# Kernel tuning notes

Hardware: AMD Instinct MI355X
Metric: run time of the kernel (lower is better)

## Reference

```python
import jax, jax.numpy as jnp
from jax import lax
import numpy as np

MB, N, QST, EPS = 512, 25, 11, 1e-5

def _coords():
    i = np.arange(25)
    # faithful to python3 true division: (i/5 - 2)/2.0, (i%5 - 2)/2.0
    c = np.stack([(i / 5 - 2) / 2.0, (i % 5 - 2) / 2.0], axis=-1).astype(np.float32)
    return jnp.asarray(c)  # [25, 2]

def _conv_bn(x, w, b, g, beta):
    # Conv2d(k=3, stride=2, pad=1) -> ReLU -> BatchNorm (training-mode batch stats)
    y = lax.conv_general_dilated(x, w, (2, 2), [(1, 1), (1, 1)],
                                 dimension_numbers=('NCHW', 'OIHW', 'NCHW'))
    y = jax.nn.relu(y + b[None, :, None, None])
    mean = y.mean(axis=(0, 2, 3), keepdims=True)
    var = y.var(axis=(0, 2, 3), keepdims=True)
    return (y - mean) * jax.lax.rsqrt(var + EPS) * g[None, :, None, None] + beta[None, :, None, None]

def setup_inputs() -> dict:
    key = jax.random.key(0)
    ks = jax.random.split(key, 20)
    w = lambda k, s: jax.random.normal(k, s, jnp.float32) * 0.05
    inp = {
        'img': jax.random.normal(ks[0], (MB, 3, 75, 75), jnp.float32),
        'qst': jax.random.normal(ks[1], (MB, QST), jnp.float32),
        'c1w': w(ks[2], (24, 3, 3, 3)),  'c1b': jnp.zeros((24,)), 'bn1g': jnp.ones((24,)), 'bn1b': jnp.zeros((24,)),
        'c2w': w(ks[3], (24, 24, 3, 3)), 'c2b': jnp.zeros((24,)), 'bn2g': jnp.ones((24,)), 'bn2b': jnp.zeros((24,)),
        'c3w': w(ks[4], (24, 24, 3, 3)), 'c3b': jnp.zeros((24,)), 'bn3g': jnp.ones((24,)), 'bn3b': jnp.zeros((24,)),
        'c4w': w(ks[5], (24, 24, 3, 3)), 'c4b': jnp.zeros((24,)), 'bn4g': jnp.ones((24,)), 'bn4b': jnp.zeros((24,)),
        'gw1': w(ks[6], (256, 63)),  'gb1': jnp.zeros((256,)),
        'gw2': w(ks[7], (256, 256)), 'gb2': jnp.zeros((256,)),
        'gw3': w(ks[8], (256, 256)), 'gb3': jnp.zeros((256,)),
        'gw4': w(ks[9], (256, 256)), 'gb4': jnp.zeros((256,)),
        'fw1': w(ks[10], (256, 256)), 'fb1': jnp.zeros((256,)),
        'fw2': w(ks[11], (256, 256)), 'fb2': jnp.zeros((256,)),
        'fw3': w(ks[12], (10, 256)),  'fb3': jnp.zeros((10,)),
    }
    return inp

def reference(img, qst, c1w, c1b, bn1g, bn1b, c2w, c2b, bn2g, bn2b,
              c3w, c3b, bn3g, bn3b, c4w, c4b, bn4g, bn4b,
              gw1, gb1, gw2, gb2, gw3, gb3, gw4, gb4,
              fw1, fb1, fw2, fb2, fw3, fb3):
    x = _conv_bn(img, c1w, c1b, bn1g, bn1b)
    x = _conv_bn(x, c2w, c2b, bn2g, bn2b)
    x = _conv_bn(x, c3w, c3b, bn3g, bn3b)
    x = _conv_bn(x, c4w, c4b, bn4g, bn4b)  # [mb, 24, 5, 5]
    mb, C = x.shape[0], x.shape[1]
    n = x.shape[2] * x.shape[3]
    xf = x.reshape(mb, C, n).transpose(0, 2, 1)              # [mb, N, 24]
    coord = jnp.broadcast_to(_coords()[None], (mb, n, 2))
    xf = jnp.concatenate([xf, coord], axis=-1)               # [mb, N, 26]
    qrep = jnp.broadcast_to(qst[:, None, :], (mb, n, QST))
    xj = jnp.concatenate([xf, qrep], axis=-1)                # [mb, N, 37]
    # pair[b,a,c] = [xf[b,c], xf[b,a], qst[b]]  (x_i varies over axis 2, x_j over axis 1)
    pair = jnp.concatenate([
        jnp.broadcast_to(xf[:, None, :, :], (mb, n, n, xf.shape[-1])),
        jnp.broadcast_to(xj[:, :, None, :], (mb, n, n, xj.shape[-1])),
    ], axis=-1)                                              # [mb, N, N, 63]
    h = pair.reshape(mb * n * n, -1)
    for w, b in ((gw1, gb1), (gw2, gb2), (gw3, gb3), (gw4, gb4)):
        h = jax.nn.relu(h @ w.T + b)
    xg = h.reshape(mb, n * n, 256).sum(axis=1)               # sum pooling over pairs
    y = jax.nn.relu(xg @ fw1.T + fb1)
    y = jax.nn.relu(y @ fw2.T + fb2)   # dropout treated as identity (eval mode)
    y = y @ fw3.T + fb3
    return jax.nn.log_softmax(y, axis=-1)
```

## Files before the change

### kernel.cpp

```cpp
#include <hip/hip_runtime.h>

typedef __bf16 bf16_t;
typedef __bf16 bf16x8 __attribute__((ext_vector_type(8)));
typedef __bf16 bf16x4 __attribute__((ext_vector_type(4)));
typedef float f32x16 __attribute__((ext_vector_type(16)));

#define MB 512
#define GROWS 96
#define GT_PER_B 7

template <int CIN, int HIN, int WIN, int HOUT, int WOUT, bool HASBN>
__global__ __launch_bounds__(256) void conv_v4(const float* __restrict__ in,
                                               const float* __restrict__ wT,
                                               const float* __restrict__ bias,
                                               const float* __restrict__ statsIn,
                                               const float* __restrict__ gIn,
                                               const float* __restrict__ bIn, float invcntIn,
                                               float* __restrict__ out,
                                               float* __restrict__ statsOut)
{
    __shared__ float red[4 * 48];
    const int NPOS = HOUT * WOUT;
    int idx = blockIdx.x * 256 + threadIdx.x;
    int n = idx / NPOS, pos = idx - n * NPOS;
    int oh = pos / WOUT, ow = pos - oh * WOUT;

    int off[9];
    bool vld[9];
#pragma unroll
    for (int kh = 0; kh < 3; ++kh) {
        int ih = 2 * oh - 1 + kh;
        bool vh = (unsigned)ih < (unsigned)HIN;
        int ihc = vh ? ih : 0;
#pragma unroll
        for (int kw = 0; kw < 3; ++kw) {
            int iw = 2 * ow - 1 + kw;
            bool vw = (unsigned)iw < (unsigned)WIN;
            vld[kh * 3 + kw] = vh && vw;
            off[kh * 3 + kw] = ihc * WIN + (vw ? iw : 0);
        }
    }

    float acc[24];
#pragma unroll
    for (int c = 0; c < 24; ++c) acc[c] = 0.f;

    const float* srcBase = in + (size_t)n * CIN * HIN * WIN;
#pragma unroll 1
    for (int ci = 0; ci < CIN; ++ci) {
        float sc, sh;
        if (HASBN) {
            float mean = statsIn[ci * 2] * invcntIn;
            float var  = statsIn[ci * 2 + 1] * invcntIn - mean * mean;
            sc = gIn[ci] * rsqrtf(var + 1e-5f);
            sh = bIn[ci] - mean * sc;
        } else { sc = 1.f; sh = 0.f; }
        const float* src = srcBase + ci * HIN * WIN;
        float iv[9];
#pragma unroll
        for (int t = 0; t < 9; ++t) {
            float raw = src[off[t]];
            iv[t] = vld[t] ? fmaf(raw, sc, sh) : 0.f;
        }
        const float* wp = wT + ci * 9 * 24;
#pragma unroll
        for (int t = 0; t < 9; ++t) {
#pragma unroll
            for (int c4 = 0; c4 < 6; ++c4) {
                float4 w4 = *(const float4*)(wp + t * 24 + c4 * 4);
                acc[c4 * 4 + 0] = fmaf(iv[t], w4.x, acc[c4 * 4 + 0]);
                acc[c4 * 4 + 1] = fmaf(iv[t], w4.y, acc[c4 * 4 + 1]);
                acc[c4 * 4 + 2] = fmaf(iv[t], w4.z, acc[c4 * 4 + 2]);
                acc[c4 * 4 + 3] = fmaf(iv[t], w4.w, acc[c4 * 4 + 3]);
            }
        }
    }

    int wv = threadIdx.x >> 6, lane = threadIdx.x & 63;
#pragma unroll
    for (int c = 0; c < 24; ++c) {
        float v = fmaxf(acc[c] + bias[c], 0.f);
        out[((size_t)(n * 24 + c) * HOUT + oh) * WOUT + ow] = v;
        float s1 = v, s2 = v * v;
#pragma unroll
        for (int o = 1; o < 64; o <<= 1) {
            s1 += __shfl_xor(s1, o);
            s2 += __shfl_xor(s2, o);
        }
        if (lane == 0) { red[wv * 48 + c * 2] = s1; red[wv * 48 + c * 2 + 1] = s2; }
    }
    __syncthreads();
    if (threadIdx.x < 48) {
        float t = red[threadIdx.x] + red[48 + threadIdx.x] + red[96 + threadIdx.x] + red[144 + threadIdx.x];
        atomicAdd(&statsOut[threadIdx.x], t);
    }
}

__global__ void build_features(const float* __restrict__ y4, const float* __restrict__ stats4,
                               const float* __restrict__ g4, const float* __restrict__ b4,
                               const float* __restrict__ qst,
                               bf16_t* __restrict__ xf26, bf16_t* __restrict__ qstb)
{
    int idx = blockIdx.x * 256 + threadIdx.x;
    if (idx < MB * 11) qstb[idx] = (bf16_t)qst[idx];
    if (idx >= MB * 25) return;
    int b = idx / 25, p = idx % 25;
    const float invcnt = 1.f / (MB * 25);
#pragma unroll
    for (int ch = 0; ch < 24; ++ch) {
        float mean = stats4[ch * 2] * invcnt;
        float var  = stats4[ch * 2 + 1] * invcnt - mean * mean;
        float s    = g4[ch] * rsqrtf(var + 1e-5f);
        float v    = s * y4[(b * 24 + ch) * 25 + p] + (b4[ch] - mean * s);
        xf26[idx * 26 + ch] = (bf16_t)v;
    }
    xf26[idx * 26 + 24] = (bf16_t)((p / 5.0f - 2.0f) * 0.5f);
    xf26[idx * 26 + 25] = (bf16_t)(((float)(p % 5) - 2.0f) * 0.5f);
}

__device__ __forceinline__ void frag256(int idx, const float* __restrict__ gw, bf16_t* __restrict__ Wf)
{
    int j = idx & 7, lane = (idx >> 3) & 63, ks = (idx >> 9) & 15, nt = idx >> 13;
    int n = nt * 32 + (lane & 31), k = ks * 16 + (lane >> 5) * 8 + j;
    Wf[idx] = (bf16_t)gw[n * 256 + k];
}

__global__ void prep_weights(const float* __restrict__ gw1, const float* __restrict__ gw2,
                             const float* __restrict__ gw3, const float* __restrict__ gw4,
                             const float* __restrict__ fw1, const float* __restrict__ fw2,
                             const float* __restrict__ c1w, const float* __restrict__ c2w,
                             const float* __restrict__ c3w, const float* __restrict__ c4w,
                             bf16_t* __restrict__ W1f, bf16_t* __restrict__ W2f,
                             bf16_t* __restrict__ W3f, bf16_t* __restrict__ W4f,
                             float* __restrict__ fw1T, float* __restrict__ fw2T,
                             float* __restrict__ wT1, float* __restrict__ wT2,
                             float* __restrict__ wT3, float* __restrict__ wT4)
{
    int idx = blockIdx.x * 256 + threadIdx.x;
    if (idx < 16384) {
        int j = idx & 7, lane = (idx >> 3) & 63, ks = (idx >> 9) & 3, nt = idx >> 11;
        int n = nt * 32 + (lane & 31), k = ks * 16 + (lane >> 5) * 8 + j;
        W1f[idx] = (k < 63) ? (bf16_t)gw1[n * 63 + k] : (bf16_t)0.0f;
        return;
    }
    idx -= 16384;
    if (idx < 65536) { frag256(idx, gw2, W2f); return; }
    idx -= 65536;
    if (idx < 65536) { frag256(idx, gw3, W3f); return; }
    idx -= 65536;
    if (idx < 65536) { frag256(idx, gw4, W4f); return; }
    idx -= 65536;
    if (idx < 65536) { int k = idx >> 8, nn = idx & 255; fw1T[idx] = fw1[nn * 256 + k]; return; }
    idx -= 65536;
    if (idx < 65536) { int k = idx >> 8, nn = idx & 255; fw2T[idx] = fw2[nn * 256 + k]; return; }
    idx -= 65536;
    if (idx < 648)   { int k = idx / 24, co = idx - k * 24; wT1[idx] = c1w[co * 27 + k]; return; }
    idx -= 648;
    if (idx < 5184)  { int k = idx / 24, co = idx - k * 24; wT2[idx] = c2w[co * 216 + k]; return; }
    idx -= 5184;
    if (idx < 5184)  { int k = idx / 24, co = idx - k * 24; wT3[idx] = c3w[co * 216 + k]; return; }
    idx -= 5184;
    if (idx < 5184)  { int k = idx / 24, co = idx - k * 24; wT4[idx] = c4w[co * 216 + k]; return; }
}

template <int NKS>
__device__ __forceinline__ void g_layer(const bf16_t* hs, const bf16_t* __restrict__ Wf,
                                        int wid, int lane, f32x16 acc[3][2])
{
    int m31 = lane & 31, half = lane >> 5;
#pragma unroll
    for (int mt = 0; mt < 3; ++mt)
#pragma unroll
        for (int nt = 0; nt < 2; ++nt) acc[mt][nt] = (f32x16)(0.f);
#pragma unroll
    for (int ks = 0; ks < NKS; ++ks) {
        int kc = ks * 2 + half;
        bf16x8 hf[3];
#pragma unroll
        for (int mt = 0; mt < 3; ++mt) {
            int m = mt * 32 + m31;
            hf[mt] = *(const bf16x8*)(hs + m * 256 + ((kc ^ m31) << 3));
        }
        bf16x8 wf[2];
#pragma unroll
        for (int nt = 0; nt < 2; ++nt)
            wf[nt] = *(const bf16x8*)(Wf + (size_t)(((wid * 2 + nt) * NKS + ks) * 64 + lane) * 8);
#pragma unroll
        for (int nt = 0; nt < 2; ++nt)
#pragma unroll
            for (int mt = 0; mt < 3; ++mt)
                acc[mt][nt] = __builtin_amdgcn_mfma_f32_32x32x16_bf16(wf[nt], hf[mt], acc[mt][nt], 0, 0, 0);
    }
}

__device__ __forceinline__ void g_store(bf16_t* hs, const float* __restrict__ bias,
                                        int wid, int lane, f32x16 acc[3][2])
{
    int m31 = lane & 31, half = lane >> 5;
#pragma unroll
    for (int mt = 0; mt < 3; ++mt) {
        int m = mt * 32 + m31;
#pragma unroll
        for (int nt = 0; nt < 2; ++nt) {
            int nbase = (wid * 2 + nt) * 32;
#pragma unroll
            for (int g = 0; g < 4; ++g) {
                int n0 = nbase + g * 8 + half * 4;
                float4 bv = *(const float4*)(bias + n0);
                bf16x4 v;
                v[0] = (bf16_t)fmaxf(acc[mt][nt][g * 4 + 0] + bv.x, 0.f);
                v[1] = (bf16_t)fmaxf(acc[mt][nt][g * 4 + 1] + bv.y, 0.f);
                v[2] = (bf16_t)fmaxf(acc[mt][nt][g * 4 + 2] + bv.z, 0.f);
                v[3] = (bf16_t)fmaxf(acc[mt][nt][g * 4 + 3] + bv.w, 0.f);
                int chunk = n0 >> 3;
                *(bf16x4*)(hs + m * 256 + ((chunk ^ m31) << 3) + (half << 2)) = v;
            }
        }
    }
}

__global__ void __launch_bounds__(256, 3)
g_mlp(const bf16_t* __restrict__ xf26, const bf16_t* __restrict__ qstb,
      const bf16_t* __restrict__ W1f, const bf16_t* __restrict__ W2f,
      const bf16_t* __restrict__ W3f, const bf16_t* __restrict__ W4f,
      const float* __restrict__ b1, const float* __restrict__ b2,
      const float* __restrict__ b3, const float* __restrict__ b4,
      float* __restrict__ xg)
{
    __shared__ __align__(16) bf16_t hs[GROWS * 256];
    int b    = blockIdx.x / GT_PER_B;
    int tile = blockIdx.x % GT_PER_B;
    int tid  = threadIdx.x;

    for (int i = tid; i < GROWS * 8; i += 256) {
        int m = i >> 3, c = i & 7;
        int p = tile * GROWS + m;
        bf16x8 v;
        if (p < 625) {
            int a = p / 25, cp = p - a * 25;
            const bf16_t* f1 = xf26 + (b * 25 + cp) * 26;
            const bf16_t* f2 = xf26 + (b * 25 + a) * 26;
            const bf16_t* f3 = qstb + b * 11;
#pragma unroll
            for (int j = 0; j < 8; ++j) {
                int col = c * 8 + j;
                bf16_t u = (bf16_t)0.0f;
                if (col < 26) u = f1[col];
                else if (col < 52) u = f2[col - 26];
                else if (col < 63) u = f3[col - 52];
                v[j] = u;
            }
        } else {
#pragma unroll
            for (int j = 0; j < 8; ++j) v[j] = (bf16_t)0.0f;
        }
        *(bf16x8*)(hs + m * 256 + ((c ^ (m & 31)) << 3)) = v;
    }
    __syncthreads();

    int wid = tid >> 6, lane = tid & 63;
    int m31 = lane & 31, half = lane >> 5;
    f32x16 acc[3][2];

    g_layer<4>(hs, W1f, wid, lane, acc);
    __syncthreads(); g_store(hs, b1, wid, lane, acc); __syncthreads();
    g_layer<16>(hs, W2f, wid, lane, acc);
    __syncthreads(); g_store(hs, b2, wid, lane, acc); __syncthreads();
    g_layer<16>(hs, W3f, wid, lane, acc);
    __syncthreads(); g_store(hs, b3, wid, lane, acc); __syncthreads();
    g_layer<16>(hs, W4f, wid, lane, acc);

#pragma unroll
    for (int nt = 0; nt < 2; ++nt) {
        int nbase = (wid * 2 + nt) * 32;
        float bf[16];
#pragma unroll
        for (int r = 0; r < 16; ++r)
            bf[r] = b4[nbase + (r & 3) + 8 * (r >> 2) + 4 * half];
        f32x16 t = (f32x16)(0.f);
#pragma unroll
        for (int mt = 0; mt < 3; ++mt) {
            int p = tile * GROWS + mt * 32 + m31;
            if (p < 625) {
#pragma unroll
                for (int r = 0; r < 16; ++r)
                    t[r] += fmaxf(acc[mt][nt][r] + bf[r], 0.f);
            }
        }
#pragma unroll
        for (int off = 1; off < 32; off <<= 1) {
#pragma unroll
            for (int r = 0; r < 16; ++r) t[r] += __shfl_xor(t[r], off);
        }
        if (m31 == 0) {
#pragma unroll
            for (int r = 0; r < 16; ++r) {
                int nn = nbase + (r & 3) + 8 * (r >> 2) + 4 * half;
                atomicAdd(&xg[b * 256 + nn], t[r]);
            }
        }
    }
}

__global__ void f_mlp(const float* __restrict__ xg, const float* __restrict__ fw1T, const float* __restrict__ fb1,
                      const float* __restrict__ fw2T, const float* __restrict__ fb2,
                      const float* __restrict__ fw3, const float* __restrict__ fb3,
                      float* __restrict__ out)
{
    __shared__ float xa[256], xb[256], lg[10];
    int b = blockIdx.x, t = threadIdx.x;
    xa[t] = xg[b * 256 + t];
    __syncthreads();
    float a = fb1[t];
    for (int k = 0; k < 256; ++k) a += fw1T[k * 256 + t] * xa[k];
    xb[t] = fmaxf(a, 0.f);
    __syncthreads();
    a = fb2[t];
    for (int k = 0; k < 256; ++k) a += fw2T[k * 256 + t] * xb[k];
    xa[t] = fmaxf(a, 0.f);
    __syncthreads();
    if (t < 10) {
        float s = fb3[t];
        for (int k = 0; k < 256; ++k) s += fw3[t * 256 + k] * xa[k];
        lg[t] = s;
    }
    __syncthreads();
    if (t == 0) {
        float m = lg[0];
        for (int i = 1; i < 10; ++i) m = fmaxf(m, lg[i]);
        float s = 0.f;
        for (int i = 0; i < 10; ++i) s += expf(lg[i] - m);
        float ls = m + logf(s);
        for (int i = 0; i < 10; ++i) out[b * 10 + i] = lg[i] - ls;
    }
}

extern "C" void kernel_launch(void* const* d_in, const int* in_sizes, int n_in,
                              void* d_out, int out_size, void* d_ws, size_t ws_size,
                              hipStream_t stream)
{
    (void)in_sizes; (void)n_in; (void)out_size; (void)ws_size;
    const float* img  = (const float*)d_in[0];
    const float* qst  = (const float*)d_in[1];
    const float* c1w  = (const float*)d_in[2];
    const float* c1b  = (const float*)d_in[3];
    const float* bn1g = (const float*)d_in[4];
    const float* bn1b = (const float*)d_in[5];
    const float* c2w  = (const float*)d_in[6];
    const float* c2b  = (const float*)d_in[7];
    const float* bn2g = (const float*)d_in[8];
    const float* bn2b = (const float*)d_in[9];
    const float* c3w  = (const float*)d_in[10];
    const float* c3b  = (const float*)d_in[11];
    const float* bn3g = (const float*)d_in[12];
    const float* bn3b = (const float*)d_in[13];
    const float* c4w  = (const float*)d_in[14];
    const float* c4b  = (const float*)d_in[15];
    const float* bn4g = (const float*)d_in[16];
    const float* bn4b = (const float*)d_in[17];
    const float* gw1  = (const float*)d_in[18];
    const float* gb1  = (const float*)d_in[19];
    const float* gw2  = (const float*)d_in[20];
    const float* gb2  = (const float*)d_in[21];
    const float* gw3  = (const float*)d_in[22];
    const float* gb3  = (const float*)d_in[23];
    const float* gw4  = (const float*)d_in[24];
    const float* gb4  = (const float*)d_in[25];
    const float* fw1  = (const float*)d_in[26];
    const float* fb1  = (const float*)d_in[27];
    const float* fw2  = (const float*)d_in[28];
    const float* fb2  = (const float*)d_in[29];
    const float* fw3  = (const float*)d_in[30];
    const float* fb3  = (const float*)d_in[31];

    const int Y1 = 512 * 24 * 38 * 38;
    const int Y2 = 512 * 24 * 19 * 19;
    const int Y3 = 512 * 24 * 10 * 10;
    const int Y4 = 512 * 24 * 5 * 5;

    float* fp = (float*)d_ws;
    float* y1    = fp;  fp += Y1;
    float* y2    = fp;  fp += Y2;
    float* y3    = fp;  fp += Y3;
    float* y4    = fp;  fp += Y4;
    float* stats = fp;  fp += 192;
    float* xg    = fp;  fp += 512 * 256;
    float* fw1T  = fp;  fp += 65536;
    float* fw2T  = fp;  fp += 65536;
    float* wT1   = fp;  fp += 648;
    float* wT2   = fp;  fp += 5184;
    float* wT3   = fp;  fp += 5184;
    float* wT4   = fp;  fp += 5184;
    bf16_t* bp   = (bf16_t*)fp;
    bf16_t* xf26 = bp;  bp += 512 * 25 * 26;
    bf16_t* qstb = bp;  bp += 512 * 11;
    bf16_t* W1f  = bp;  bp += 16384;
    bf16_t* W2f  = bp;  bp += 65536;
    bf16_t* W3f  = bp;  bp += 65536;
    bf16_t* W4f  = bp;  bp += 65536;

    hipMemsetAsync(stats, 0, 192 * sizeof(float), stream);
    hipMemsetAsync(xg, 0, 512 * 256 * sizeof(float), stream);

    prep_weights<<<1408, 256, 0, stream>>>(gw1, gw2, gw3, gw4, fw1, fw2, c1w, c2w, c3w, c4w,
                                           W1f, W2f, W3f, W4f, fw1T, fw2T,
                                           wT1, wT2, wT3, wT4);

    conv_v4<3, 75, 75, 38, 38, false><<<2888, 256, 0, stream>>>(
        img, wT1, c1b, nullptr, nullptr, nullptr, 0.f, y1, stats + 0);

    conv_v4<24, 38, 38, 19, 19, true><<<722, 256, 0, stream>>>(
        y1, wT2, c2b, stats + 0, bn1g, bn1b, 1.f / (512.f * 1444.f), y2, stats + 48);

    conv_v4<24, 19, 19, 10, 10, true><<<200, 256, 0, stream>>>(
        y2, wT3, c3b, stats + 48, bn2g, bn2b, 1.f / (512.f * 361.f), y3, stats + 96);

    conv_v4<24, 10, 10, 5, 5, true><<<50, 256, 0, stream>>>(
        y3, wT4, c4b, stats + 96, bn3g, bn3b, 1.f / (512.f * 100.f), y4, stats + 144);

    build_features<<<50, 256, 0, stream>>>(y4, stats + 144, bn4g, bn4b, qst, xf26, qstb);

    g_mlp<<<512 * GT_PER_B, 256, 0, stream>>>(xf26, qstb, W1f, W2f, W3f, W4f,
                                              gb1, gb2, gb3, gb4, xg);

    f_mlp<<<512, 256, 0, stream>>>(xg, fw1T, fb1, fw2T, fb2, fw3, fb3, (float*)d_out);
}
```

Before: 619.5 us.

## Split conv output channels across waves to quadruple conv parallelism

Each conv block now covers 64 output positions, and its four waves each compute 6 of the 24 output channels instead of one thread computing all 24. This gives four times as many blocks and fewer accumulator registers per thread, which should help the small late conv layers fill the GPU. In exchange, every input value is loaded by four waves instead of one, and more atomic stat reductions are issued.

```diff
diff --git a/kernel.cpp b/kernel.cpp
--- a/kernel.cpp
+++ b/kernel.cpp
@@ -10,18 +10,21 @@
 #define GT_PER_B 7
 
 template <int CIN, int HIN, int WIN, int HOUT, int WOUT, bool HASBN>
-__global__ __launch_bounds__(256) void conv_v4(const float* __restrict__ in,
-                                               const float* __restrict__ wT,
-                                               const float* __restrict__ bias,
-                                               const float* __restrict__ statsIn,
-                                               const float* __restrict__ gIn,
-                                               const float* __restrict__ bIn, float invcntIn,
-                                               float* __restrict__ out,
-                                               float* __restrict__ statsOut)
-{
-    __shared__ float red[4 * 48];
+__global__ __launch_bounds__(256) void conv_v4b(const float* __restrict__ in,
+                                                const float* __restrict__ wT,
+                                                const float* __restrict__ bias,
+                                                const float* __restrict__ statsIn,
+                                                const float* __restrict__ gIn,
+                                                const float* __restrict__ bIn, float invcntIn,
+                                                float* __restrict__ out,
+                                                float* __restrict__ statsOut)
+{
+    __shared__ float red[48];
     const int NPOS = HOUT * WOUT;
-    int idx = blockIdx.x * 256 + threadIdx.x;
+    int lane = threadIdx.x & 63;
+    int cg   = threadIdx.x >> 6;
+    int co0  = cg * 6;
+    int idx  = blockIdx.x * 64 + lane;
     int n = idx / NPOS, pos = idx - n * NPOS;
     int oh = pos / WOUT, ow = pos - oh * WOUT;
 
@@ -41,9 +44,9 @@
         }
     }
 
-    float acc[24];
-#pragma unroll
-    for (int c = 0; c < 24; ++c) acc[c] = 0.f;
+    float acc[6];
+#pragma unroll
+    for (int c = 0; c < 6; ++c) acc[c] = 0.f;
 
     const float* srcBase = in + (size_t)n * CIN * HIN * WIN;
 #pragma unroll 1
@@ -62,38 +65,35 @@
             float raw = src[off[t]];
             iv[t] = vld[t] ? fmaf(raw, sc, sh) : 0.f;
         }
-        const float* wp = wT + ci * 9 * 24;
+        const float* wp = wT + ci * 9 * 24 + co0;
 #pragma unroll
         for (int t = 0; t < 9; ++t) {
-#pragma unroll
-            for (int c4 = 0; c4 < 6; ++c4) {
-                float4 w4 = *(const float4*)(wp + t * 24 + c4 * 4);
-                acc[c4 * 4 + 0] = fmaf(iv[t], w4.x, acc[c4 * 4 + 0]);
-                acc[c4 * 4 + 1] = fmaf(iv[t], w4.y, acc[c4 * 4 + 1]);
-                acc[c4 * 4 + 2] = fmaf(iv[t], w4.z, acc[c4 * 4 + 2]);
-                acc[c4 * 4 + 3] = fmaf(iv[t], w4.w, acc[c4 * 4 + 3]);
-            }
-        }
-    }
-
-    int wv = threadIdx.x >> 6, lane = threadIdx.x & 63;
-#pragma unroll
-    for (int c = 0; c < 24; ++c) {
-        float v = fmaxf(acc[c] + bias[c], 0.f);
-        out[((size_t)(n * 24 + c) * HOUT + oh) * WOUT + ow] = v;
+            float2 w01 = *(const float2*)(wp + t * 24);
+            float2 w23 = *(const float2*)(wp + t * 24 + 2);
+            float2 w45 = *(const float2*)(wp + t * 24 + 4);
+            acc[0] = fmaf(iv[t], w01.x, acc[0]);
+            acc[1] = fmaf(iv[t], w01.y, acc[1]);
+            acc[2] = fmaf(iv[t], w23.x, acc[2]);
+            acc[3] = fmaf(iv[t], w23.y, acc[3]);
+            acc[4] = fmaf(iv[t], w45.x, acc[4]);
+            acc[5] = fmaf(iv[t], w45.y, acc[5]);
+        }
+    }
+
+#pragma unroll
+    for (int c = 0; c < 6; ++c) {
+        float v = fmaxf(acc[c] + bias[co0 + c], 0.f);
+        out[(size_t)(n * 24 + co0 + c) * NPOS + pos] = v;
         float s1 = v, s2 = v * v;
 #pragma unroll
         for (int o = 1; o < 64; o <<= 1) {
             s1 += __shfl_xor(s1, o);
             s2 += __shfl_xor(s2, o);
         }
-        if (lane == 0) { red[wv * 48 + c * 2] = s1; red[wv * 48 + c * 2 + 1] = s2; }
-    }
-    __syncthreads();
-    if (threadIdx.x < 48) {
-        float t = red[threadIdx.x] + red[48 + threadIdx.x] + red[96 + threadIdx.x] + red[144 + threadIdx.x];
-        atomicAdd(&statsOut[threadIdx.x], t);
-    }
+        if (lane == 0) { red[(co0 + c) * 2] = s1; red[(co0 + c) * 2 + 1] = s2; }
+    }
+    __syncthreads();
+    if (threadIdx.x < 48) atomicAdd(&statsOut[threadIdx.x], red[threadIdx.x]);
 }
 
 __global__ void build_features(const float* __restrict__ y4, const float* __restrict__ stats4,
@@ -406,16 +406,16 @@
                                            W1f, W2f, W3f, W4f, fw1T, fw2T,
                                            wT1, wT2, wT3, wT4);
 
-    conv_v4<3, 75, 75, 38, 38, false><<<2888, 256, 0, stream>>>(
+    conv_v4b<3, 75, 75, 38, 38, false><<<11552, 256, 0, stream>>>(
         img, wT1, c1b, nullptr, nullptr, nullptr, 0.f, y1, stats + 0);
 
-    conv_v4<24, 38, 38, 19, 19, true><<<722, 256, 0, stream>>>(
+    conv_v4b<24, 38, 38, 19, 19, true><<<2888, 256, 0, stream>>>(
         y1, wT2, c2b, stats + 0, bn1g, bn1b, 1.f / (512.f * 1444.f), y2, stats + 48);
 
-    conv_v4<24, 19, 19, 10, 10, true><<<200, 256, 0, stream>>>(
+    conv_v4b<24, 19, 19, 10, 10, true><<<800, 256, 0, stream>>>(
         y2, wT3, c3b, stats + 48, bn2g, bn2b, 1.f / (512.f * 361.f), y3, stats + 96);
 
-    conv_v4<24, 10, 10, 5, 5, true><<<50, 256, 0, stream>>>(
+    conv_v4b<24, 10, 10, 5, 5, true><<<200, 256, 0, stream>>>(
         y3, wT4, c4b, stats + 96, bn3g, bn3b, 1.f / (512.f * 100.f), y4, stats + 144);
 
     build_features<<<50, 256, 0, stream>>>(y4, stats + 144, bn4g, bn4b, qst, xf26, qstb);
```

Result: slower. 976.3 us (+57.6%).

## Split conv input channels across waves and reduce partial sums in shared memory

Applied to the files above, without the earlier changes.

Conv layers 2-4 now split the input-channel loop across S groups of waves. Each block covers fewer output positions, so the grid gets more blocks and the small later layers get more parallelism. Partial accumulators are reduced through a 25 KB shared buffer before bias, ReLU, output and BN statistics. This adds an extra barrier and shared-memory traffic, and the large LDS footprint may limit occupancy. It also changes the wave-to-channel mapping used for the stats reduction.

```diff
diff --git a/kernel.cpp b/kernel.cpp
--- a/kernel.cpp
+++ b/kernel.cpp
@@ -9,8 +9,8 @@
 #define GROWS 96
 #define GT_PER_B 7
 
-template <int CIN, int HIN, int WIN, int HOUT, int WOUT, bool HASBN>
-__global__ __launch_bounds__(256) void conv_v4(const float* __restrict__ in,
+template <int CIN, int HIN, int WIN, int HOUT, int WOUT, int S, bool HASBN>
+__global__ __launch_bounds__(256) void conv_v5(const float* __restrict__ in,
                                                const float* __restrict__ wT,
                                                const float* __restrict__ bias,
                                                const float* __restrict__ statsIn,
@@ -19,11 +19,23 @@
                                                float* __restrict__ out,
                                                float* __restrict__ statsOut)
 {
-    __shared__ float red[4 * 48];
+    constexpr int CPG = CIN / S;
+    constexpr int P   = 256 / S;
+    constexpr int CH  = 24 / S;
+    constexpr int WPG = 4 / S;
+    __shared__ float red[256 * 25];
+    __shared__ float red2[4 * 48];
+
     const int NPOS = HOUT * WOUT;
-    int idx = blockIdx.x * 256 + threadIdx.x;
+    int tid = threadIdx.x;
+    int w = tid >> 6, lane = tid & 63;
+    int cig = w / WPG;
+    int pos_local = (w % WPG) * 64 + lane;
+    int idx = blockIdx.x * P + pos_local;
     int n = idx / NPOS, pos = idx - n * NPOS;
     int oh = pos / WOUT, ow = pos - oh * WOUT;
+
+    if (tid < 192) red2[tid] = 0.f;
 
     int off[9];
     bool vld[9];
@@ -47,7 +59,8 @@
 
     const float* srcBase = in + (size_t)n * CIN * HIN * WIN;
 #pragma unroll 1
-    for (int ci = 0; ci < CIN; ++ci) {
+    for (int cio = 0; cio < CPG; ++cio) {
+        int ci = cig * CPG + cio;
         float sc, sh;
         if (HASBN) {
             float mean = statsIn[ci * 2] * invcntIn;
@@ -76,23 +89,36 @@
         }
     }
 
-    int wv = threadIdx.x >> 6, lane = threadIdx.x & 63;
-#pragma unroll
-    for (int c = 0; c < 24; ++c) {
-        float v = fmaxf(acc[c] + bias[c], 0.f);
-        out[((size_t)(n * 24 + c) * HOUT + oh) * WOUT + ow] = v;
+    {
+        float* pr = red + (cig * P + pos_local) * 25;
+#pragma unroll
+        for (int c = 0; c < 24; ++c) pr[c] = acc[c];
+    }
+    __syncthreads();
+
+    int g2 = tid / P, pos2 = tid % P;
+    int idx2 = blockIdx.x * P + pos2;
+    int n2 = idx2 / NPOS, posg = idx2 - n2 * NPOS;
+#pragma unroll
+    for (int c = 0; c < CH; ++c) {
+        int ch = g2 * CH + c;
+        float v = 0.f;
+#pragma unroll
+        for (int s = 0; s < S; ++s) v += red[(s * P + pos2) * 25 + ch];
+        v = fmaxf(v + bias[ch], 0.f);
+        out[(size_t)(n2 * 24 + ch) * NPOS + posg] = v;
         float s1 = v, s2 = v * v;
 #pragma unroll
         for (int o = 1; o < 64; o <<= 1) {
             s1 += __shfl_xor(s1, o);
             s2 += __shfl_xor(s2, o);
         }
-        if (lane == 0) { red[wv * 48 + c * 2] = s1; red[wv * 48 + c * 2 + 1] = s2; }
-    }
-    __syncthreads();
-    if (threadIdx.x < 48) {
-        float t = red[threadIdx.x] + red[48 + threadIdx.x] + red[96 + threadIdx.x] + red[144 + threadIdx.x];
-        atomicAdd(&statsOut[threadIdx.x], t);
+        if (lane == 0) { red2[w * 48 + ch * 2] = s1; red2[w * 48 + ch * 2 + 1] = s2; }
+    }
+    __syncthreads();
+    if (tid < 48) {
+        float t = red2[tid] + red2[48 + tid] + red2[96 + tid] + red2[144 + tid];
+        atomicAdd(&statsOut[tid], t);
     }
 }
 
@@ -406,16 +432,16 @@
                                            W1f, W2f, W3f, W4f, fw1T, fw2T,
                                            wT1, wT2, wT3, wT4);
 
-    conv_v4<3, 75, 75, 38, 38, false><<<2888, 256, 0, stream>>>(
+    conv_v5<3, 75, 75, 38, 38, 1, false><<<2888, 256, 0, stream>>>(
         img, wT1, c1b, nullptr, nullptr, nullptr, 0.f, y1, stats + 0);
 
-    conv_v4<24, 38, 38, 19, 19, true><<<722, 256, 0, stream>>>(
+    conv_v5<24, 38, 38, 19, 19, 2, true><<<1444, 256, 0, stream>>>(
         y1, wT2, c2b, stats + 0, bn1g, bn1b, 1.f / (512.f * 1444.f), y2, stats + 48);
 
-    conv_v4<24, 19, 19, 10, 10, true><<<200, 256, 0, stream>>>(
+    conv_v5<24, 19, 19, 10, 10, 4, true><<<800, 256, 0, stream>>>(
         y2, wT3, c3b, stats + 48, bn2g, bn2b, 1.f / (512.f * 361.f), y3, stats + 96);
 
-    conv_v4<24, 10, 10, 5, 5, true><<<50, 256, 0, stream>>>(
+    conv_v5<24, 10, 10, 5, 5, 4, true><<<200, 256, 0, stream>>>(
         y3, wT4, c4b, stats + 96, bn3g, bn3b, 1.f / (512.f * 100.f), y4, stats + 144);
 
     build_features<<<50, 256, 0, stream>>>(y4, stats + 144, bn4g, bn4b, qst, xf26, qstb);
```

After: 666.7 us. 1.08x slower.
